# Kernel optimization log

Hardware: AMD Instinct MI355X
Metric: run time of the kernel (lower is better)

## Reference

```python
import jax, jax.numpy as jnp
import numpy as np

N_ATOM, N_QUERY, KNN = 100000, 20000, 32
E = N_QUERY * KNN
HID, EDGE_F, HEADS = 128, 16, 8
D_HEAD = HID // HEADS
LN_EPS = 1e-5


def setup_inputs() -> dict:
    key = jax.random.key(0)
    ks = jax.random.split(key, 16)
    s = 1.0 / np.sqrt(HID)
    src = jax.random.randint(ks[0], (E,), 0, N_ATOM)
    dst = jnp.repeat(jnp.arange(N_QUERY), KNN)  # each query has KNN incoming edges
    return {
        "h_atom": jax.random.normal(ks[1], (N_ATOM, HID), jnp.float32),
        "h_query": jax.random.normal(ks[2], (N_QUERY, HID), jnp.float32),
        "edge_attr": jax.random.uniform(ks[3], (E, EDGE_F), jnp.float32),
        "W_q": jax.random.normal(ks[4], (HID, HID), jnp.float32) * s,
        "W_k": jax.random.normal(ks[5], (HID, HID), jnp.float32) * s,
        "W_v": jax.random.normal(ks[6], (HID, HID), jnp.float32) * s,
        "W_rbf": jax.random.normal(ks[7], (HEADS, EDGE_F), jnp.float32) * (1.0 / np.sqrt(EDGE_F)),
        "W1": jax.random.normal(ks[8], (HID, 2 * HID), jnp.float32) * (1.0 / np.sqrt(2 * HID)),
        "b1": jnp.zeros((HID,), jnp.float32),
        "W2": jax.random.normal(ks[9], (HID, HID), jnp.float32) * s,
        "b2": jnp.zeros((HID,), jnp.float32),
        "ln_gamma": jnp.ones((HID,), jnp.float32),
        "ln_beta": jnp.zeros((HID,), jnp.float32),
        "edge_index": jnp.stack([src, dst]),
        "n_query": N_QUERY,
    }


def reference(h_atom, h_query, edge_attr, W_q, W_k, W_v, W_rbf, W1, b1, W2, b2,
              ln_gamma, ln_beta, edge_index, n_query):
    src, dst = edge_index[0], edge_index[1]
    En = src.shape[0]
    # gather + project, per-edge multi-head Q/K/V  [E, H, d]
    Q = (h_query[dst] @ W_q.T).reshape(En, HEADS, D_HEAD)
    K = (h_atom[src] @ W_k.T).reshape(En, HEADS, D_HEAD)
    V = (h_atom[src] @ W_v.T).reshape(En, HEADS, D_HEAD)
    scores = jnp.einsum("ehd,ehd->eh", Q, K) / np.sqrt(D_HEAD) + edge_attr @ W_rbf.T  # [E,H]
    # segment softmax over edges sharing the same dst query, per head
    seg_max = jax.lax.stop_gradient(jax.ops.segment_max(scores, dst, num_segments=n_query))
    ex = jnp.exp(scores - seg_max[dst])
    denom = jax.ops.segment_sum(ex, dst, num_segments=n_query)
    alpha = ex / (denom[dst] + 1e-16)  # [E,H]
    # weighted scatter-add aggregation
    msgs = (alpha[:, :, None] * V).reshape(En, HID)
    agg = jax.ops.segment_sum(msgs, dst, num_segments=n_query)  # [Nq, HID]
    # update MLP + residual + LayerNorm
    z = jnp.concatenate([h_query, agg], axis=-1)
    delta = jax.nn.relu(z @ W1.T + b1) @ W2.T + b2
    y = h_query + delta
    mu = y.mean(-1, keepdims=True)
    var = y.var(-1, keepdims=True)
    return (y - mu) / jnp.sqrt(var + LN_EPS) * ln_gamma + ln_beta
```

## Files before the change

kernel.cpp:

```cpp
#include <hip/hip_runtime.h>
#include <hip/hip_bf16.h>
#include <math.h>

#define N_ATOM   100000
#define N_QUERY  20000
#define KNN      32

typedef __attribute__((ext_vector_type(8))) short  short8;
typedef __attribute__((ext_vector_type(4))) float  floatx4;
typedef __attribute__((ext_vector_type(2))) float  fx2;

static __device__ __forceinline__ unsigned short f2bf_bits(float f) {
  union { __hip_bfloat16 h; unsigned short u; } cv;
  cv.h = __float2bfloat16(f);
  return cv.u;
}
static __device__ __forceinline__ float bflo(unsigned int u) { return __uint_as_float(u << 16); }
static __device__ __forceinline__ float bfhi(unsigned int u) { return __uint_as_float(u & 0xffff0000u); }

__global__ void pack_all_kernel(const float* __restrict__ Wq, const float* __restrict__ Wk,
                                const float* __restrict__ Wv, const float* __restrict__ W1,
                                const float* __restrict__ W2,
                                unsigned short* __restrict__ WKVp, unsigned short* __restrict__ WQp,
                                unsigned short* __restrict__ W1p,  unsigned short* __restrict__ W2p) {
  int tid = blockIdx.x * blockDim.x + threadIdx.x;
  if (tid >= 98304) return;
  const float *Wa, *Wb; int nsplit, Kd, Nd; unsigned short* dst; float scale = 1.0f;
  int t = tid;
  if (t < 32768)      { Wa = Wk; Wb = Wv; nsplit = 128; Kd = 128; Nd = 256; dst = WKVp; }
  else if (t < 49152) { t -= 32768; Wa = Wq; Wb = Wq; nsplit = 128; Kd = 128; Nd = 128; dst = WQp; scale = 0.25f; }
  else if (t < 81920) { t -= 49152; Wa = W1; Wb = W1; nsplit = 128; Kd = 256; Nd = 128; dst = W1p; }
  else                { t -= 81920; Wa = W2; Wb = W2; nsplit = 128; Kd = 128; Nd = 128; dst = W2p; }
  int j    = t & 7;
  int lane = (t >> 3) & 63;
  int t2   = t >> 9;
  int NT   = Nd >> 4;
  int ntile = t2 % NT;
  int ktile = t2 / NT;
  int k = ktile * 32 + (lane >> 4) * 8 + j;
  int n = ntile * 16 + (lane & 15);
  float v = (n < nsplit) ? Wa[(size_t)n * Kd + k] : Wb[(size_t)(n - nsplit) * Kd + k];
  dst[t] = f2bf_bits(v * scale);
}

__global__ __launch_bounds__(256) void gemm_kvq(
    const float* __restrict__ h_atom, const float* __restrict__ h_query,
    const unsigned short* __restrict__ WKVp, const unsigned short* __restrict__ WQp,
    unsigned char* __restrict__ Kp8, unsigned char* __restrict__ Vp8,
    unsigned short* __restrict__ Qb) {
  constexpr int KB = (N_ATOM + 63) / 64;
  __shared__ char lds[16384];
  const int l    = threadIdx.x & 63;
  const int w    = threadIdx.x >> 6;
  const int quad = l >> 4;
  const int col0 = l & 15;

  if ((int)blockIdx.x < KB) {
    const int row0 = blockIdx.x * 64 + w * 16;
    int arow = row0 + col0;
    if (arow >= N_ATOM) arow = N_ATOM - 1;
    floatx4 acc[16];
#pragma unroll
    for (int i = 0; i < 16; i++) acc[i] = (floatx4){0.f, 0.f, 0.f, 0.f};
    const float* aptr = h_atom + (size_t)arow * 128 + quad * 8;
#pragma unroll
    for (int k0 = 0; k0 < 128; k0 += 32) {
      floatx4 a0 = *(const floatx4*)(aptr + k0);
      floatx4 a1 = *(const floatx4*)(aptr + k0 + 4);
      short8 af;
      af[0] = (short)f2bf_bits(a0[0]); af[1] = (short)f2bf_bits(a0[1]);
      af[2] = (short)f2bf_bits(a0[2]); af[3] = (short)f2bf_bits(a0[3]);
      af[4] = (short)f2bf_bits(a1[0]); af[5] = (short)f2bf_bits(a1[1]);
      af[6] = (short)f2bf_bits(a1[2]); af[7] = (short)f2bf_bits(a1[3]);
      const unsigned short* bbase = WKVp + (size_t)(k0 >> 5) * 16 * 512 + l * 8;
#pragma unroll
      for (int nt = 0; nt < 16; nt++) {
        short8 bf = *(const short8*)(bbase + nt * 512);
        acc[nt] = __builtin_amdgcn_mfma_f32_16x16x32_bf16(af, bf, acc[nt], 0, 0, 0);
      }
    }
#pragma unroll
    for (int nt = 0; nt < 16; nt++) {
#pragma unroll
      for (int r = 0; r < 4; r++) {
        int rl = w * 16 + quad * 4 + r;
        int c  = nt * 16 + col0;
        int pk = __builtin_amdgcn_cvt_pk_fp8_f32(acc[nt][r], acc[nt][r], 0, false);
        if (c < 128) lds[rl * 128 + c] = (char)(pk & 0xff);
        else         lds[8192 + rl * 128 + (c - 128)] = (char)(pk & 0xff);
      }
    }
    __syncthreads();
    const int row0g = blockIdx.x * 64;
#pragma unroll
    for (int it = 0; it < 2; it++) {
      int off = threadIdx.x * 16 + it * 4096;
      if (row0g + (off >> 7) < N_ATOM)
        *(float4*)(Kp8 + (size_t)row0g * 128 + off) = *(const float4*)&lds[off];
    }
#pragma unroll
    for (int it = 0; it < 2; it++) {
      int off = threadIdx.x * 16 + it * 4096;
      if (row0g + (off >> 7) < N_ATOM)
        *(float4*)(Vp8 + (size_t)row0g * 128 + off) = *(const float4*)&lds[8192 + off];
    }
  } else {
    const int row0 = ((int)blockIdx.x - KB) * 64 + w * 16;
    int arow = row0 + col0;
    if (arow >= N_QUERY) arow = N_QUERY - 1;
    floatx4 acc[8];
#pragma unroll
    for (int i = 0; i < 8; i++) acc[i] = (floatx4){0.f, 0.f, 0.f, 0.f};
    const float* aptr = h_query + (size_t)arow * 128 + quad * 8;
#pragma unroll
    for (int k0 = 0; k0 < 128; k0 += 32) {
      floatx4 a0 = *(const floatx4*)(aptr + k0);
      floatx4 a1 = *(const floatx4*)(aptr + k0 + 4);
      short8 af;
      af[0] = (short)f2bf_bits(a0[0]); af[1] = (short)f2bf_bits(a0[1]);
      af[2] = (short)f2bf_bits(a0[2]); af[3] = (short)f2bf_bits(a0[3]);
      af[4] = (short)f2bf_bits(a1[0]); af[5] = (short)f2bf_bits(a1[1]);
      af[6] = (short)f2bf_bits(a1[2]); af[7] = (short)f2bf_bits(a1[3]);
      const unsigned short* bbase = WQp + (size_t)(k0 >> 5) * 8 * 512 + l * 8;
#pragma unroll
      for (int nt = 0; nt < 8; nt++) {
        short8 bf = *(const short8*)(bbase + nt * 512);
        acc[nt] = __builtin_amdgcn_mfma_f32_16x16x32_bf16(af, bf, acc[nt], 0, 0, 0);
      }
    }
#pragma unroll
    for (int nt = 0; nt < 8; nt++) {
#pragma unroll
      for (int r = 0; r < 4; r++) {
        int row = row0 + quad * 4 + r;
        if (row < N_QUERY) Qb[(size_t)row * 128 + nt * 16 + col0] = f2bf_bits(acc[nt][r]);
      }
    }
  }
}

__global__ __launch_bounds__(256) void attn_kernel(
    const unsigned short* __restrict__ Qb,
    const unsigned char* __restrict__ Kp8,
    const unsigned char* __restrict__ Vp8,
    const float* __restrict__ edge_attr,
    const float* __restrict__ Wrbf,
    const int* __restrict__ src,
    float* __restrict__ Agg) {
  const int l = threadIdx.x & 63;
  const int w = threadIdx.x >> 6;
  const int q = blockIdx.x * 4 + w;
  const int j = l >> 3;
  const int h = l & 7;

  const int e0 = q * KNN;
  int srcj = (l < KNN) ? src[e0 + l] : 0;

  float qd[16];
  {
    const unsigned int* qp = (const unsigned int*)(Qb + (size_t)q * 128 + h * 16);
#pragma unroll
    for (int i = 0; i < 8; i++) {
      unsigned int u = qp[i];
      qd[2 * i] = bflo(u); qd[2 * i + 1] = bfhi(u);
    }
  }
  float wr[16];
  {
    const float* wp = Wrbf + h * 16;
#pragma unroll
    for (int i = 0; i < 16; i++) wr[i] = wp[i];
  }

  float acc[16];
#pragma unroll
  for (int i = 0; i < 16; i++) acc[i] = 0.f;
  float lsum = 0.f;

#pragma unroll
  for (int p = 0; p < 4; p++) {
    const int e = p * 8 + j;
    int s = __shfl(srcj, e, 64);
    uint4 kq = *(const uint4*)(Kp8 + (size_t)s * 128 + h * 16);
    uint4 vq = *(const uint4*)(Vp8 + (size_t)s * 128 + h * 16);
    const float4* ep = (const float4*)(edge_attr + (size_t)(e0 + e) * 16);
    float4 ea0 = ep[0], ea1 = ep[1], ea2 = ep[2], ea3 = ep[3];

    float kd = 0.f;
    {
      fx2 f0, f1;
      f0 = __builtin_amdgcn_cvt_pk_f32_fp8((int)kq.x, false);
      f1 = __builtin_amdgcn_cvt_pk_f32_fp8((int)kq.x, true);
      kd += qd[0] * f0[0] + qd[1] * f0[1] + qd[2] * f1[0] + qd[3] * f1[1];
      f0 = __builtin_amdgcn_cvt_pk_f32_fp8((int)kq.y, false);
      f1 = __builtin_amdgcn_cvt_pk_f32_fp8((int)kq.y, true);
      kd += qd[4] * f0[0] + qd[5] * f0[1] + qd[6] * f1[0] + qd[7] * f1[1];
      f0 = __builtin_amdgcn_cvt_pk_f32_fp8((int)kq.z, false);
      f1 = __builtin_amdgcn_cvt_pk_f32_fp8((int)kq.z, true);
      kd += qd[8] * f0[0] + qd[9] * f0[1] + qd[10] * f1[0] + qd[11] * f1[1];
      f0 = __builtin_amdgcn_cvt_pk_f32_fp8((int)kq.w, false);
      f1 = __builtin_amdgcn_cvt_pk_f32_fp8((int)kq.w, true);
      kd += qd[12] * f0[0] + qd[13] * f0[1] + qd[14] * f1[0] + qd[15] * f1[1];
    }
    float ed = wr[0]*ea0.x + wr[1]*ea0.y + wr[2]*ea0.z + wr[3]*ea0.w
             + wr[4]*ea1.x + wr[5]*ea1.y + wr[6]*ea1.z + wr[7]*ea1.w
             + wr[8]*ea2.x + wr[9]*ea2.y + wr[10]*ea2.z + wr[11]*ea2.w
             + wr[12]*ea3.x + wr[13]*ea3.y + wr[14]*ea3.z + wr[15]*ea3.w;

    float pe = __expf(kd + ed);
    lsum += pe;
    {
      fx2 g0, g1;
      g0 = __builtin_amdgcn_cvt_pk_f32_fp8((int)vq.x, false);
      g1 = __builtin_amdgcn_cvt_pk_f32_fp8((int)vq.x, true);
      acc[0] += pe * g0[0]; acc[1] += pe * g0[1]; acc[2] += pe * g1[0]; acc[3] += pe * g1[1];
      g0 = __builtin_amdgcn_cvt_pk_f32_fp8((int)vq.y, false);
      g1 = __builtin_amdgcn_cvt_pk_f32_fp8((int)vq.y, true);
      acc[4] += pe * g0[0]; acc[5] += pe * g0[1]; acc[6] += pe * g1[0]; acc[7] += pe * g1[1];
      g0 = __builtin_amdgcn_cvt_pk_f32_fp8((int)vq.z, false);
      g1 = __builtin_amdgcn_cvt_pk_f32_fp8((int)vq.z, true);
      acc[8] += pe * g0[0]; acc[9] += pe * g0[1]; acc[10] += pe * g1[0]; acc[11] += pe * g1[1];
      g0 = __builtin_amdgcn_cvt_pk_f32_fp8((int)vq.w, false);
      g1 = __builtin_amdgcn_cvt_pk_f32_fp8((int)vq.w, true);
      acc[12] += pe * g0[0]; acc[13] += pe * g0[1]; acc[14] += pe * g1[0]; acc[15] += pe * g1[1];
    }
  }

#pragma unroll
  for (int mask = 8; mask <= 32; mask <<= 1) {
    lsum += __shfl_xor(lsum, mask, 64);
#pragma unroll
    for (int i = 0; i < 16; i++) acc[i] += __shfl_xor(acc[i], mask, 64);
  }
  float inv = 1.f / (lsum + 1e-16f);
  float* dst = Agg + (size_t)q * 128 + h * 16;
  if (j == 0) {
    float4 o0 = {acc[0] * inv, acc[1] * inv, acc[2] * inv, acc[3] * inv};
    float4 o1 = {acc[4] * inv, acc[5] * inv, acc[6] * inv, acc[7] * inv};
    *(float4*)(dst)     = o0;
    *(float4*)(dst + 4) = o1;
  } else if (j == 1) {
    float4 o2 = {acc[8] * inv, acc[9] * inv, acc[10] * inv, acc[11] * inv};
    float4 o3 = {acc[12] * inv, acc[13] * inv, acc[14] * inv, acc[15] * inv};
    *(float4*)(dst + 8)  = o2;
    *(float4*)(dst + 12) = o3;
  }
}

__global__ __launch_bounds__(256) void mlp_kernel(
    const float* __restrict__ h_query, const float* __restrict__ Agg,
    const unsigned short* __restrict__ W1p, const unsigned short* __restrict__ W2p,
    const float* __restrict__ b1, const float* __restrict__ b2,
    const float* __restrict__ gamma, const float* __restrict__ beta,
    float* __restrict__ out) {
  constexpr int M = N_QUERY;
  constexpr int STRIDE = 136;
  __shared__ unsigned short hid[64 * STRIDE];

  const int l    = threadIdx.x & 63;
  const int w    = threadIdx.x >> 6;
  const int quad = l >> 4;
  const int col0 = l & 15;
  const int row0 = blockIdx.x * 64 + w * 16;
  int arow = row0 + col0;
  if (arow >= M) arow = M - 1;

  floatx4 acc[8];
#pragma unroll
  for (int i = 0; i < 8; i++) acc[i] = (floatx4){0.f, 0.f, 0.f, 0.f};
#pragma unroll
  for (int k0 = 0; k0 < 256; k0 += 32) {
    const float* sp = (k0 < 128) ? (h_query + (size_t)arow * 128 + k0)
                                 : (Agg + (size_t)arow * 128 + (k0 - 128));
    floatx4 a0 = *(const floatx4*)(sp + quad * 8);
    floatx4 a1 = *(const floatx4*)(sp + quad * 8 + 4);
    short8 af;
    af[0] = (short)f2bf_bits(a0[0]); af[1] = (short)f2bf_bits(a0[1]);
    af[2] = (short)f2bf_bits(a0[2]); af[3] = (short)f2bf_bits(a0[3]);
    af[4] = (short)f2bf_bits(a1[0]); af[5] = (short)f2bf_bits(a1[1]);
    af[6] = (short)f2bf_bits(a1[2]); af[7] = (short)f2bf_bits(a1[3]);
    const unsigned short* bbase = W1p + (size_t)(k0 >> 5) * 8 * 512 + l * 8;
#pragma unroll
    for (int nt = 0; nt < 8; nt++) {
      short8 bf = *(const short8*)(bbase + nt * 512);
      acc[nt] = __builtin_amdgcn_mfma_f32_16x16x32_bf16(af, bf, acc[nt], 0, 0, 0);
    }
  }
#pragma unroll
  for (int nt = 0; nt < 8; nt++) {
#pragma unroll
    for (int r = 0; r < 4; r++) {
      int rl = w * 16 + quad * 4 + r;
      float v = acc[nt][r] + b1[nt * 16 + col0];
      hid[rl * STRIDE + nt * 16 + col0] = f2bf_bits(fmaxf(v, 0.f));
    }
  }
  __syncthreads();

  floatx4 acc2[8];
#pragma unroll
  for (int i = 0; i < 8; i++) acc2[i] = (floatx4){0.f, 0.f, 0.f, 0.f};
  const int rloc = w * 16 + col0;
#pragma unroll
  for (int k0 = 0; k0 < 128; k0 += 32) {
    short8 af = *(const short8*)(hid + rloc * STRIDE + k0 + quad * 8);
    const unsigned short* bbase = W2p + (size_t)(k0 >> 5) * 8 * 512 + l * 8;
#pragma unroll
    for (int nt = 0; nt < 8; nt++) {
      short8 bf = *(const short8*)(bbase + nt * 512);
      acc2[nt] = __builtin_amdgcn_mfma_f32_16x16x32_bf16(af, bf, acc2[nt], 0, 0, 0);
    }
  }

#pragma unroll
  for (int r = 0; r < 4; r++) {
    int row = row0 + quad * 4 + r;
    int rr  = row < M ? row : M - 1;
    float v[8];
    float s1 = 0.f, s2 = 0.f;
#pragma unroll
    for (int nt = 0; nt < 8; nt++) {
      int c = nt * 16 + col0;
      v[nt] = acc2[nt][r] + b2[c] + h_query[(size_t)rr * 128 + c];
      s1 += v[nt];
    }
    s1 += __shfl_xor(s1, 1, 64); s1 += __shfl_xor(s1, 2, 64);
    s1 += __shfl_xor(s1, 4, 64); s1 += __shfl_xor(s1, 8, 64);
#pragma unroll
    for (int nt = 0; nt < 8; nt++) s2 += v[nt] * v[nt];
    s2 += __shfl_xor(s2, 1, 64); s2 += __shfl_xor(s2, 2, 64);
    s2 += __shfl_xor(s2, 4, 64); s2 += __shfl_xor(s2, 8, 64);
    float mean = s1 * (1.0f / 128.0f);
    float var  = s2 * (1.0f / 128.0f) - mean * mean;
    float rstd = rsqrtf(var + 1e-5f);
    if (row < M) {
#pragma unroll
      for (int nt = 0; nt < 8; nt++) {
        int c = nt * 16 + col0;
        out[(size_t)row * 128 + c] = (v[nt] - mean) * rstd * gamma[c] + beta[c];
      }
    }
  }
}

extern "C" void kernel_launch(void* const* d_in, const int* in_sizes, int n_in,
                              void* d_out, int out_size, void* d_ws, size_t ws_size,
                              hipStream_t stream) {
  const float* h_atom    = (const float*)d_in[0];
  const float* h_query   = (const float*)d_in[1];
  const float* edge_attr = (const float*)d_in[2];
  const float* W_q  = (const float*)d_in[3];
  const float* W_k  = (const float*)d_in[4];
  const float* W_v  = (const float*)d_in[5];
  const float* Wrbf = (const float*)d_in[6];
  const float* W1   = (const float*)d_in[7];
  const float* b1   = (const float*)d_in[8];
  const float* W2   = (const float*)d_in[9];
  const float* b2   = (const float*)d_in[10];
  const float* ln_g = (const float*)d_in[11];
  const float* ln_b = (const float*)d_in[12];
  const int* edge_index = (const int*)d_in[13];
  float* out = (float*)d_out;

  char* ws = (char*)d_ws;
  unsigned char*  Kp8 = (unsigned char*)(ws);
  unsigned char*  Vp8 = (unsigned char*)(ws + 12800000);
  unsigned short* Qb  = (unsigned short*)(ws + 25600000);
  float* Agg          = (float*)(ws + 30720000);
  unsigned short* WKVp = (unsigned short*)(ws + 40960000);
  unsigned short* WQp  = WKVp + 32768;
  unsigned short* W1p  = WQp  + 16384;
  unsigned short* W2p  = W1p  + 32768;

  pack_all_kernel<<<(98304 + 255) / 256, 256, 0, stream>>>(
      W_q, W_k, W_v, W1, W2, WKVp, WQp, W1p, W2p);

  constexpr int KB = (N_ATOM + 63) / 64;
  constexpr int QB = (N_QUERY + 63) / 64;
  gemm_kvq<<<KB + QB, 256, 0, stream>>>(h_atom, h_query, WKVp, WQp, Kp8, Vp8, Qb);

  attn_kernel<<<N_QUERY / 4, 256, 0, stream>>>(Qb, Kp8, Vp8, edge_attr, Wrbf, edge_index, Agg);

  mlp_kernel<<<(N_QUERY + 63) / 64, 256, 0, stream>>>(
      h_query, Agg, W1p, W2p, b1, b2, ln_g, ln_b, out);
}
```

Before: 218.1 us.

## Interleave K/V fp8 rows and retile KV GEMM into 2x2 warp grid

New measurement: 238.9 us. 9.5% more time.

```diff
diff --git a/kernel.cpp b/kernel.cpp
--- a/kernel.cpp
+++ b/kernel.cpp
@@ -46,8 +46,7 @@
 __global__ __launch_bounds__(256) void gemm_kvq(
     const float* __restrict__ h_atom, const float* __restrict__ h_query,
     const unsigned short* __restrict__ WKVp, const unsigned short* __restrict__ WQp,
-    unsigned char* __restrict__ Kp8, unsigned char* __restrict__ Vp8,
-    unsigned short* __restrict__ Qb) {
+    unsigned char* __restrict__ KVp8, unsigned short* __restrict__ Qb) {
   constexpr int KB = (N_ATOM + 63) / 64;
   __shared__ char lds[16384];
   const int l    = threadIdx.x & 63;
@@ -56,53 +55,62 @@
   const int col0 = l & 15;
 
   if ((int)blockIdx.x < KB) {
-    const int row0 = blockIdx.x * 64 + w * 16;
-    int arow = row0 + col0;
-    if (arow >= N_ATOM) arow = N_ATOM - 1;
-    floatx4 acc[16];
-#pragma unroll
-    for (int i = 0; i < 16; i++) acc[i] = (floatx4){0.f, 0.f, 0.f, 0.f};
-    const float* aptr = h_atom + (size_t)arow * 128 + quad * 8;
+    const int rg = w >> 1;
+    const int cg = w & 1;
+    const int rowb = blockIdx.x * 64;
+    int arow[2];
+#pragma unroll
+    for (int mt = 0; mt < 2; mt++) {
+      int r = rowb + rg * 32 + mt * 16 + col0;
+      arow[mt] = (r < N_ATOM) ? r : (N_ATOM - 1);
+    }
+    floatx4 acc[2][8];
+#pragma unroll
+    for (int mt = 0; mt < 2; mt++)
+#pragma unroll
+      for (int nt = 0; nt < 8; nt++) acc[mt][nt] = (floatx4){0.f, 0.f, 0.f, 0.f};
+
 #pragma unroll
     for (int k0 = 0; k0 < 128; k0 += 32) {
-      floatx4 a0 = *(const floatx4*)(aptr + k0);
-      floatx4 a1 = *(const floatx4*)(aptr + k0 + 4);
-      short8 af;
-      af[0] = (short)f2bf_bits(a0[0]); af[1] = (short)f2bf_bits(a0[1]);
-      af[2] = (short)f2bf_bits(a0[2]); af[3] = (short)f2bf_bits(a0[3]);
-      af[4] = (short)f2bf_bits(a1[0]); af[5] = (short)f2bf_bits(a1[1]);
-      af[6] = (short)f2bf_bits(a1[2]); af[7] = (short)f2bf_bits(a1[3]);
-      const unsigned short* bbase = WKVp + (size_t)(k0 >> 5) * 16 * 512 + l * 8;
-#pragma unroll
-      for (int nt = 0; nt < 16; nt++) {
+      short8 af[2];
+#pragma unroll
+      for (int mt = 0; mt < 2; mt++) {
+        const float* ap = h_atom + (size_t)arow[mt] * 128 + k0 + quad * 8;
+        floatx4 a0 = *(const floatx4*)(ap);
+        floatx4 a1 = *(const floatx4*)(ap + 4);
+        af[mt][0] = (short)f2bf_bits(a0[0]); af[mt][1] = (short)f2bf_bits(a0[1]);
+        af[mt][2] = (short)f2bf_bits(a0[2]); af[mt][3] = (short)f2bf_bits(a0[3]);
+        af[mt][4] = (short)f2bf_bits(a1[0]); af[mt][5] = (short)f2bf_bits(a1[1]);
+        af[mt][6] = (short)f2bf_bits(a1[2]); af[mt][7] = (short)f2bf_bits(a1[3]);
+      }
+      const unsigned short* bbase = WKVp + ((size_t)(k0 >> 5) * 16 + cg * 8) * 512 + l * 8;
+#pragma unroll
+      for (int nt = 0; nt < 8; nt++) {
         short8 bf = *(const short8*)(bbase + nt * 512);
-        acc[nt] = __builtin_amdgcn_mfma_f32_16x16x32_bf16(af, bf, acc[nt], 0, 0, 0);
-      }
-    }
-#pragma unroll
-    for (int nt = 0; nt < 16; nt++) {
-#pragma unroll
-      for (int r = 0; r < 4; r++) {
-        int rl = w * 16 + quad * 4 + r;
-        int c  = nt * 16 + col0;
-        int pk = __builtin_amdgcn_cvt_pk_fp8_f32(acc[nt][r], acc[nt][r], 0, false);
-        if (c < 128) lds[rl * 128 + c] = (char)(pk & 0xff);
-        else         lds[8192 + rl * 128 + (c - 128)] = (char)(pk & 0xff);
+#pragma unroll
+        for (int mt = 0; mt < 2; mt++)
+          acc[mt][nt] = __builtin_amdgcn_mfma_f32_16x16x32_bf16(af[mt], bf, acc[mt][nt], 0, 0, 0);
+      }
+    }
+#pragma unroll
+    for (int mt = 0; mt < 2; mt++) {
+#pragma unroll
+      for (int nt = 0; nt < 8; nt++) {
+#pragma unroll
+        for (int r = 0; r < 4; r++) {
+          int rl = rg * 32 + mt * 16 + quad * 4 + r;
+          int c  = cg * 128 + nt * 16 + col0;
+          int pk = __builtin_amdgcn_cvt_pk_fp8_f32(acc[mt][nt][r], acc[mt][nt][r], 0, false);
+          lds[rl * 256 + c] = (char)(pk & 0xff);
+        }
       }
     }
     __syncthreads();
-    const int row0g = blockIdx.x * 64;
-#pragma unroll
-    for (int it = 0; it < 2; it++) {
+#pragma unroll
+    for (int it = 0; it < 4; it++) {
       int off = threadIdx.x * 16 + it * 4096;
-      if (row0g + (off >> 7) < N_ATOM)
-        *(float4*)(Kp8 + (size_t)row0g * 128 + off) = *(const float4*)&lds[off];
-    }
-#pragma unroll
-    for (int it = 0; it < 2; it++) {
-      int off = threadIdx.x * 16 + it * 4096;
-      if (row0g + (off >> 7) < N_ATOM)
-        *(float4*)(Vp8 + (size_t)row0g * 128 + off) = *(const float4*)&lds[8192 + off];
+      if (rowb + (off >> 8) < N_ATOM)
+        *(float4*)(KVp8 + (size_t)rowb * 256 + off) = *(const float4*)&lds[off];
     }
   } else {
     const int row0 = ((int)blockIdx.x - KB) * 64 + w * 16;
@@ -141,8 +149,7 @@
 
 __global__ __launch_bounds__(256) void attn_kernel(
     const unsigned short* __restrict__ Qb,
-    const unsigned char* __restrict__ Kp8,
-    const unsigned char* __restrict__ Vp8,
+    const unsigned char* __restrict__ KVp8,
     const float* __restrict__ edge_attr,
     const float* __restrict__ Wrbf,
     const int* __restrict__ src,
@@ -154,7 +161,9 @@
   const int h = l & 7;
 
   const int e0 = q * KNN;
-  int srcj = (l < KNN) ? src[e0 + l] : 0;
+  int s_arr[4];
+#pragma unroll
+  for (int p = 0; p < 4; p++) s_arr[p] = src[e0 + p * 8 + j];
 
   float qd[16];
   {
@@ -180,9 +189,9 @@
 #pragma unroll
   for (int p = 0; p < 4; p++) {
     const int e = p * 8 + j;
-    int s = __shfl(srcj, e, 64);
-    uint4 kq = *(const uint4*)(Kp8 + (size_t)s * 128 + h * 16);
-    uint4 vq = *(const uint4*)(Vp8 + (size_t)s * 128 + h * 16);
+    const unsigned char* bp = KVp8 + (size_t)s_arr[p] * 256;
+    uint4 kq = *(const uint4*)(bp + h * 16);
+    uint4 vq = *(const uint4*)(bp + 128 + h * 16);
     const float4* ep = (const float4*)(edge_attr + (size_t)(e0 + e) * 16);
     float4 ea0 = ep[0], ea1 = ep[1], ea2 = ep[2], ea3 = ep[3];
 
@@ -363,10 +372,9 @@
   float* out = (float*)d_out;
 
   char* ws = (char*)d_ws;
-  unsigned char*  Kp8 = (unsigned char*)(ws);
-  unsigned char*  Vp8 = (unsigned char*)(ws + 12800000);
-  unsigned short* Qb  = (unsigned short*)(ws + 25600000);
-  float* Agg          = (float*)(ws + 30720000);
+  unsigned char*  KVp8 = (unsigned char*)(ws);
+  unsigned short* Qb   = (unsigned short*)(ws + 25600000);
+  float* Agg           = (float*)(ws + 30720000);
   unsigned short* WKVp = (unsigned short*)(ws + 40960000);
   unsigned short* WQp  = WKVp + 32768;
   unsigned short* W1p  = WQp  + 16384;
@@ -377,9 +385,9 @@
 
   constexpr int KB = (N_ATOM + 63) / 64;
   constexpr int QB = (N_QUERY + 63) / 64;
-  gemm_kvq<<<KB + QB, 256, 0, stream>>>(h_atom, h_query, WKVp, WQp, Kp8, Vp8, Qb);
-
-  attn_kernel<<<N_QUERY / 4, 256, 0, stream>>>(Qb, Kp8, Vp8, edge_attr, Wrbf, edge_index, Agg);
+  gemm_kvq<<<KB + QB, 256, 0, stream>>>(h_atom, h_query, WKVp, WQp, KVp8, Qb);
+
+  attn_kernel<<<N_QUERY / 4, 256, 0, stream>>>(Qb, KVp8, edge_attr, Wrbf, edge_index, Agg);
 
   mlp_kernel<<<(N_QUERY + 63) / 64, 256, 0, stream>>>(
       h_query, Agg, W1p, W2p, b1, b2, ln_g, ln_b, out);
```
